# Kernel tuning notes

Hardware: AMD Instinct MI355X
Metric: run time of the kernel (lower is better)

The kernel has to match this reference:

```python
import jax, jax.numpy as jnp
import numpy as np

E = 256
H = 8
DK = E // H


def setup_inputs() -> dict:
    key = jax.random.key(0)
    ks = jax.random.split(key, 16)
    B, NA, NB = 2, 2048, 2048
    x_a = jax.random.normal(ks[0], (B, NA, E), dtype=jnp.float32)
    x_b = jax.random.normal(ks[1], (B, NB, E), dtype=jnp.float32)
    s = 1.0 / np.sqrt(E)  # kaiming-normal-ish scale
    inp = {"x_a": x_a, "x_b": x_b}
    names = ["wq", "wk_a", "wk_b", "wv_a", "wv_b", "w"]
    for i, n in enumerate(names):
        inp[n + "_w"] = jax.random.normal(ks[2 + 2 * i], (E, E), dtype=jnp.float32) * s
        inp[n + "_b"] = jax.random.normal(ks[3 + 2 * i], (E,), dtype=jnp.float32) * 0.01
    return inp


def _linear(x, w, b):
    # torch nn.Linear: y = x @ w.T + b
    return jnp.einsum('bne,fe->bnf', x, w) + b


def _heads(x):
    # [B, N, E] -> [B, H, N, DK]
    B, N, _ = x.shape
    return x.reshape(B, N, H, DK).transpose(0, 2, 1, 3)


def reference(x_a, x_b, wq_w, wq_b, wk_a_w, wk_a_b, wk_b_w, wk_b_b,
              wv_a_w, wv_a_b, wv_b_w, wv_b_b, w_w, w_b):
    B, NA, _ = x_a.shape
    q = _heads(_linear(x_a, wq_w, wq_b))          # [B,H,NA,DK]
    k_a = _heads(_linear(x_a, wk_a_w, wk_a_b))    # [B,H,NA,DK]
    v_a = _heads(_linear(x_a, wv_a_w, wv_a_b))
    k_b = _heads(_linear(x_b, wk_b_w, wk_b_b))    # [B,H,NB,DK]
    v_b = _heads(_linear(x_b, wv_b_w, wv_b_b))
    k = jnp.concatenate([k_a, k_b], axis=2)       # [B,H,NA+NB,DK]
    v = jnp.concatenate([v_a, v_b], axis=2)
    scores = jnp.einsum('bhqd,bhkd->bhqk', q, k) / jnp.sqrt(jnp.float32(DK))
    p = jax.nn.softmax(scores, axis=-1)           # [B,H,NA,NA+NB]
    z = jnp.einsum('bhqk,bhkd->bhqd', p, v)       # [B,H,NA,DK]
    z = z.transpose(0, 2, 1, 3).reshape(B, NA, E)
    out = _linear(z, w_w, w_b) + x_a
    return out
```

## Files before the change

### kernel.cpp

```cpp
#include <hip/hip_runtime.h>
#include <cstdint>

typedef short bf16x8 __attribute__((ext_vector_type(8)));
typedef float f32x4 __attribute__((ext_vector_type(4)));
typedef unsigned short u16;
typedef unsigned int u32;

#define DEVI static __device__ __forceinline__


DEVI u16 f2bf(float f) {
  u32 x = __builtin_bit_cast(u32, f);
  x += 0x7fffu + ((x >> 16) & 1u);
  return (u16)(x >> 16);
}

DEVI u32 pack_bf2(float lo, float hi) {
  return (u32)f2bf(lo) | ((u32)f2bf(hi) << 16);
}

DEVI u32 cvt_pk_bf16(float lo, float hi) {
  u32 r;
  asm("v_cvt_pk_bf16_f32 %0, %1, %2" : "=v"(r) : "v"(lo), "v"(hi));
  return r;
}

DEVI f32x4 mfma16(bf16x8 a, bf16x8 b, f32x4 c) {
  return __builtin_amdgcn_mfma_f32_16x16x32_bf16(a, b, c, 0, 0, 0);
}

DEVI void load_lds16(const void* g, void* l) {
  __builtin_amdgcn_global_load_lds(
      (const __attribute__((address_space(1))) u32*)g,
      (__attribute__((address_space(3))) u32*)l, 16, 0, 0);
}

#define CSCALE 0.2550351f

DEVI int rho(int k) {
  return ((k >> 5) << 5) | (((k >> 2) & 1) << 4) | (((k >> 3) & 3) << 2) | (k & 3);
}

__global__ __launch_bounds__(256) void convert_kernel(
    const float* __restrict__ xa, const float* __restrict__ xb,
    const float* __restrict__ w0, const float* __restrict__ w1,
    const float* __restrict__ w2, const float* __restrict__ w3,
    const float* __restrict__ w4, const float* __restrict__ w5,
    u16* __restrict__ dst) {
  int i = (int)(blockIdx.x * 256u + threadIdx.x) * 8;
  const float* s;
  if (i < 1048576) {
    s = xa + i;
  } else if (i < 2097152) {
    s = xb + (i - 1048576);
  } else {
    int t = i - 2097152;
    int j = t >> 16, o = t & 65535;
    s = (j == 0 ? w0 : j == 1 ? w1 : j == 2 ? w2 : j == 3 ? w3 : j == 4 ? w4 : w5) + o;
  }
  float4 a = *(const float4*)s;
  float4 b = *(const float4*)(s + 4);
  uint4 o4;
  o4.x = pack_bf2(a.x, a.y);
  o4.y = pack_bf2(a.z, a.w);
  o4.z = pack_bf2(b.x, b.y);
  o4.w = pack_bf2(b.z, b.w);
  *(uint4*)(dst + i) = o4;
}

__global__ __launch_bounds__(256) void proj_kernel(
    const u16* __restrict__ xa_bf, const u16* __restrict__ xb_bf,
    const u16* __restrict__ wbase,
    const float* __restrict__ b0, const float* __restrict__ b1,
    const float* __restrict__ b2, const float* __restrict__ b3,
    const float* __restrict__ b4,
    u16* __restrict__ Qo, u16* __restrict__ Ko, u16* __restrict__ Vo) {
  int job = blockIdx.z;
  const u16* A = (job <= 2) ? xa_bf : xb_bf;
  const u16* W = wbase + job * 65536;
  const float* bias = job == 0 ? b0 : job == 1 ? b1 : job == 2 ? b2 : job == 3 ? b3 : b4;
  int mode = (job == 0) ? 0 : (job == 1 || job == 3) ? 1 : 2;
  int soff = (job >= 3) ? 2048 : 0;

  int tid = threadIdx.x, wid = tid >> 6, lane = tid & 63, g = lane >> 4, c = lane & 15;
  int m0 = blockIdx.x * 64, n0 = blockIdx.y * 64;
  const u16* Ap = A + (m0 + wid * 16 + c) * 256 + g * 8;
  const u16* Wp = W + (n0 + c) * 256 + g * 8;
  f32x4 acc[4] = {};
#pragma unroll
  for (int kk = 0; kk < 256; kk += 32) {
    bf16x8 af = *(const bf16x8*)(Ap + kk);
#pragma unroll
    for (int nt = 0; nt < 4; ++nt) {
      bf16x8 bfr = *(const bf16x8*)(Wp + nt * 4096 + kk);
      acc[nt] = mfma16(af, bfr, acc[nt]);
    }
  }
#pragma unroll
  for (int nt = 0; nt < 4; ++nt) {
    int f = n0 + nt * 16 + c;
    float bv = bias[f];
    int h = f >> 5, d = f & 31;
#pragma unroll
    for (int r = 0; r < 4; ++r) {
      int m = m0 + wid * 16 + g * 4 + r;
      int bq = m >> 11, n = m & 2047;
      int bh = bq * 8 + h;
      float y = acc[nt][r] + bv;
      if (mode == 0) {
        Qo[(bh * 2048 + n) * 32 + d] = f2bf(y * CSCALE);
      } else if (mode == 1) {
        int nk = soff + n;
        int pr = (nk & ~63) | rho(nk & 63);
        Ko[((size_t)bh * 4096 + pr) * 32 + d] = f2bf(y);
      } else {
        int nk = soff + n;
        Vo[(size_t)bh * 131072 + (nk >> 6) * 2048 + ((nk >> 3) & 7) * 256 +
           d * 8 + (nk & 7)] = f2bf(y);
      }
    }
  }
}

__global__ __launch_bounds__(256) void attn_kernel(
    const u16* __restrict__ Q, const u16* __restrict__ K,
    const u16* __restrict__ Vt, float* __restrict__ Zp, float* __restrict__ S) {
  __shared__ __align__(16) unsigned char sbuf[24576];
  int bid = blockIdx.x;
  int xcd = bid & 7, slot = bid >> 3;
  int bh = (xcd << 1) | (slot & 1);
  int rem = slot >> 1;
  int ks = rem & 1, qi = rem >> 1;
  int tid = threadIdx.x, wid = tid >> 6, lane = tid & 63;
  int g = lane >> 4, c = lane & 15;
  int qbase = qi * 64 + wid * 16;

  const unsigned char* Kb =
      (const unsigned char*)K + ((size_t)bh * 4096 + ks * 2048) * 64;
  const unsigned char* Vb =
      (const unsigned char*)Vt + (size_t)bh * 262144 + (size_t)ks * 131072;

  bf16x8 qf = *(const bf16x8*)(Q + ((size_t)bh * 2048 + qbase + c) * 32 + g * 8);

  int kaddr = c * 64 + ((g ^ ((c >> 1) & 3)) << 4);
  int vaddr = g * 512 + c * 16;

  int o = wid * 1024 + (lane << 4);
  int ko_src = o ^ (((o >> 7) & 3) << 4);

  f32x4 z0 = {}, z1 = {};
  float lsum = 0.f;

  load_lds16(Kb + ko_src, sbuf + wid * 1024);
  load_lds16(Vb + o, sbuf + 12288 + wid * 1024);

  int cur = 0;
  for (int t = 0; t < 32; ++t) {
    int nxt = cur + 1;
    if (nxt == 3) nxt = 0;
    if (t + 1 < 32) {
      load_lds16(Kb + (t + 1) * 4096 + ko_src, sbuf + nxt * 4096 + wid * 1024);
      load_lds16(Vb + (t + 1) * 4096 + o, sbuf + 12288 + nxt * 4096 + wid * 1024);
      __builtin_amdgcn_sched_barrier(0);
      asm volatile("s_waitcnt vmcnt(2)" ::: "memory");
    } else {
      __builtin_amdgcn_sched_barrier(0);
      asm volatile("s_waitcnt vmcnt(0)" ::: "memory");
    }
    __builtin_amdgcn_s_barrier();
    __builtin_amdgcn_sched_barrier(0);

    const unsigned char* kbuf = sbuf + cur * 4096;
    const unsigned char* vbuf = sbuf + 12288 + cur * 4096;

    bf16x8 kf0 = *(const bf16x8*)(kbuf + kaddr);
    bf16x8 kf1 = *(const bf16x8*)(kbuf + kaddr + 1024);
    bf16x8 kf2 = *(const bf16x8*)(kbuf + kaddr + 2048);
    bf16x8 kf3 = *(const bf16x8*)(kbuf + kaddr + 3072);
    bf16x8 vf00 = *(const bf16x8*)(vbuf + vaddr);
    bf16x8 vf01 = *(const bf16x8*)(vbuf + vaddr + 2048);
    bf16x8 vf10 = *(const bf16x8*)(vbuf + vaddr + 256);
    bf16x8 vf11 = *(const bf16x8*)(vbuf + vaddr + 2048 + 256);

    f32x4 zz = {};
    __builtin_amdgcn_s_setprio(1);
    f32x4 s0 = mfma16(kf0, qf, zz);
    f32x4 s1 = mfma16(kf1, qf, zz);
    f32x4 s2 = mfma16(kf2, qf, zz);
    f32x4 s3 = mfma16(kf3, qf, zz);
    __builtin_amdgcn_s_setprio(0);

    float e0[4], e1[4], e2[4], e3[4];
#pragma unroll
    for (int r = 0; r < 4; ++r) {
      e0[r] = __builtin_amdgcn_exp2f(s0[r]);
      e1[r] = __builtin_amdgcn_exp2f(s1[r]);
      e2[r] = __builtin_amdgcn_exp2f(s2[r]);
      e3[r] = __builtin_amdgcn_exp2f(s3[r]);
    }
    lsum += ((e0[0] + e0[1]) + (e0[2] + e0[3])) + ((e1[0] + e1[1]) + (e1[2] + e1[3])) +
            ((e2[0] + e2[1]) + (e2[2] + e2[3])) + ((e3[0] + e3[1]) + (e3[2] + e3[3]));

    union { u32 u[4]; bf16x8 v; } A0, A1;
    A0.u[0] = cvt_pk_bf16(e0[0], e0[1]);
    A0.u[1] = cvt_pk_bf16(e0[2], e0[3]);
    A0.u[2] = cvt_pk_bf16(e1[0], e1[1]);
    A0.u[3] = cvt_pk_bf16(e1[2], e1[3]);
    A1.u[0] = cvt_pk_bf16(e2[0], e2[1]);
    A1.u[1] = cvt_pk_bf16(e2[2], e2[3]);
    A1.u[2] = cvt_pk_bf16(e3[0], e3[1]);
    A1.u[3] = cvt_pk_bf16(e3[2], e3[3]);

    __builtin_amdgcn_s_setprio(1);
    z0 = mfma16(A0.v, vf00, z0);
    z0 = mfma16(A1.v, vf01, z0);
    z1 = mfma16(A0.v, vf10, z1);
    z1 = mfma16(A1.v, vf11, z1);
    __builtin_amdgcn_s_setprio(0);
    cur = nxt;
  }

  lsum += __shfl_xor(lsum, 16);
  lsum += __shfl_xor(lsum, 32);

  size_t zrow = ((size_t)ks * 16 + bh) * 2048;
  if (lane < 16) S[zrow + qbase + lane] = lsum;
#pragma unroll
  for (int r = 0; r < 4; ++r) {
    int m = qbase + g * 4 + r;
    float* zp = Zp + (zrow + m) * 32;
    zp[c] = z0[r];
    zp[16 + c] = z1[r];
  }
}

__global__ __launch_bounds__(256) void out_kernel(
    const float* __restrict__ Zp, const float* __restrict__ S,
    const u16* __restrict__ W, const float* __restrict__ bias,
    const float* __restrict__ resid, float* __restrict__ out) {
  int tid = threadIdx.x, wid = tid >> 6, lane = tid & 63, g = lane >> 4, c = lane & 15;
  int m0 = blockIdx.x * 16;
  int mrow = m0 + c;
  int bq = mrow >> 11, n = mrow & 2047;
  const u16* Wp = W + (wid * 64 + c) * 256 + g * 8;
  f32x4 acc[4] = {};
#pragma unroll
  for (int h = 0; h < 8; ++h) {
    int bh = bq * 8 + h;
    const float* za = Zp + ((size_t)bh * 2048 + n) * 32 + g * 8;
    const float* zb = za + (size_t)16 * 2048 * 32;
    float4 a0 = *(const float4*)za;
    float4 a1 = *(const float4*)(za + 4);
    float4 b0 = *(const float4*)zb;
    float4 b1 = *(const float4*)(zb + 4);
    float inv = 1.0f / (S[(size_t)bh * 2048 + n] + S[(size_t)(16 + bh) * 2048 + n]);
    union { u32 u[4]; bf16x8 v; } cv;
    cv.u[0] = pack_bf2((a0.x + b0.x) * inv, (a0.y + b0.y) * inv);
    cv.u[1] = pack_bf2((a0.z + b0.z) * inv, (a0.w + b0.w) * inv);
    cv.u[2] = pack_bf2((a1.x + b1.x) * inv, (a1.y + b1.y) * inv);
    cv.u[3] = pack_bf2((a1.z + b1.z) * inv, (a1.w + b1.w) * inv);
    bf16x8 af = cv.v;
#pragma unroll
    for (int nt = 0; nt < 4; ++nt) {
      bf16x8 bfr = *(const bf16x8*)(Wp + nt * 4096 + h * 32);
      acc[nt] = mfma16(af, bfr, acc[nt]);
    }
  }
#pragma unroll
  for (int nt = 0; nt < 4; ++nt) {
    int f = wid * 64 + nt * 16 + c;
    float bv = bias[f];
#pragma unroll
    for (int r = 0; r < 4; ++r) {
      int m = m0 + g * 4 + r;
      out[(size_t)m * 256 + f] = acc[nt][r] + bv + resid[(size_t)m * 256 + f];
    }
  }
}

extern "C" void kernel_launch(void* const* d_in, const int* in_sizes, int n_in,
                              void* d_out, int out_size, void* d_ws, size_t ws_size,
                              hipStream_t stream) {
  const float* xa = (const float*)d_in[0];
  const float* xb = (const float*)d_in[1];
  const float* wq_w = (const float*)d_in[2];
  const float* wq_b = (const float*)d_in[3];
  const float* wka_w = (const float*)d_in[4];
  const float* wka_b = (const float*)d_in[5];
  const float* wkb_w = (const float*)d_in[6];
  const float* wkb_b = (const float*)d_in[7];
  const float* wva_w = (const float*)d_in[8];
  const float* wva_b = (const float*)d_in[9];
  const float* wvb_w = (const float*)d_in[10];
  const float* wvb_b = (const float*)d_in[11];
  const float* w_w = (const float*)d_in[12];
  const float* w_b = (const float*)d_in[13];

  u16* ws = (u16*)d_ws;
  u16* xa_bf = ws;
  u16* xb_bf = ws + 1048576;
  u16* wbf = ws + 2097152;
  u16* Qb = ws + 2490368;
  u16* Kb = ws + 3538944;
  u16* Vtb = ws + 5636096;
  float* Zp = (float*)(ws + 7733248);
  float* S = (float*)((char*)d_ws + 23855104);

  convert_kernel<<<1216, 256, 0, stream>>>(xa, xb, wq_w, wka_w, wva_w, wkb_w,
                                           wvb_w, w_w, ws);
  proj_kernel<<<dim3(64, 4, 5), 256, 0, stream>>>(
      xa_bf, xb_bf, wbf, wq_b, wka_b, wva_b, wkb_b, wvb_b, Qb, Kb, Vtb);
  attn_kernel<<<1024, 256, 0, stream>>>(Qb, Kb, Vtb, Zp, S);
  out_kernel<<<256, 256, 0, stream>>>(Zp, S, wbf + 5 * 65536, w_b, xa,
                                      (float*)d_out);
}
```

Before: 78.35 us.

## Fuse activation conversion into projection, split attention keys four ways, MFMA row sums

Activations are no longer pre-converted to bf16 in a separate pass. The projection kernel now reads fp32 inputs and converts them in registers, so the convert kernel only handles weights. The attention kernel splits keys into four chunks instead of two, doubling the block count, and switches to a 4-deep LDS ring with prefetch distance two. Softmax row sums are now computed with an extra MFMA against a ones vector instead of VALU adds and shuffles. The output kernel merges four partials and splits the output columns across two blocks, at the cost of more partial-sum traffic and reduction work.

New measurement: 88.84 us. 1.13x slower.

```diff
diff --git a/kernel.cpp b/kernel.cpp
--- a/kernel.cpp
+++ b/kernel.cpp
@@ -42,22 +42,14 @@
 }
 
 __global__ __launch_bounds__(256) void convert_kernel(
-    const float* __restrict__ xa, const float* __restrict__ xb,
     const float* __restrict__ w0, const float* __restrict__ w1,
     const float* __restrict__ w2, const float* __restrict__ w3,
     const float* __restrict__ w4, const float* __restrict__ w5,
     u16* __restrict__ dst) {
   int i = (int)(blockIdx.x * 256u + threadIdx.x) * 8;
-  const float* s;
-  if (i < 1048576) {
-    s = xa + i;
-  } else if (i < 2097152) {
-    s = xb + (i - 1048576);
-  } else {
-    int t = i - 2097152;
-    int j = t >> 16, o = t & 65535;
-    s = (j == 0 ? w0 : j == 1 ? w1 : j == 2 ? w2 : j == 3 ? w3 : j == 4 ? w4 : w5) + o;
-  }
+  int j = i >> 16, oo = i & 65535;
+  const float* s =
+      (j == 0 ? w0 : j == 1 ? w1 : j == 2 ? w2 : j == 3 ? w3 : j == 4 ? w4 : w5) + oo;
   float4 a = *(const float4*)s;
   float4 b = *(const float4*)(s + 4);
   uint4 o4;
@@ -69,14 +61,14 @@
 }
 
 __global__ __launch_bounds__(256) void proj_kernel(
-    const u16* __restrict__ xa_bf, const u16* __restrict__ xb_bf,
+    const float* __restrict__ xa, const float* __restrict__ xb,
     const u16* __restrict__ wbase,
     const float* __restrict__ b0, const float* __restrict__ b1,
     const float* __restrict__ b2, const float* __restrict__ b3,
     const float* __restrict__ b4,
     u16* __restrict__ Qo, u16* __restrict__ Ko, u16* __restrict__ Vo) {
   int job = blockIdx.z;
-  const u16* A = (job <= 2) ? xa_bf : xb_bf;
+  const float* A = (job <= 2) ? xa : xb;
   const u16* W = wbase + job * 65536;
   const float* bias = job == 0 ? b0 : job == 1 ? b1 : job == 2 ? b2 : job == 3 ? b3 : b4;
   int mode = (job == 0) ? 0 : (job == 1 || job == 3) ? 1 : 2;
@@ -84,16 +76,22 @@
 
   int tid = threadIdx.x, wid = tid >> 6, lane = tid & 63, g = lane >> 4, c = lane & 15;
   int m0 = blockIdx.x * 64, n0 = blockIdx.y * 64;
-  const u16* Ap = A + (m0 + wid * 16 + c) * 256 + g * 8;
+  const float* Ap = A + (size_t)(m0 + wid * 16 + c) * 256 + g * 8;
   const u16* Wp = W + (n0 + c) * 256 + g * 8;
   f32x4 acc[4] = {};
 #pragma unroll
   for (int kk = 0; kk < 256; kk += 32) {
-    bf16x8 af = *(const bf16x8*)(Ap + kk);
+    float4 x0 = *(const float4*)(Ap + kk);
+    float4 x1 = *(const float4*)(Ap + kk + 4);
+    union { u32 u[4]; bf16x8 v; } af;
+    af.u[0] = cvt_pk_bf16(x0.x, x0.y);
+    af.u[1] = cvt_pk_bf16(x0.z, x0.w);
+    af.u[2] = cvt_pk_bf16(x1.x, x1.y);
+    af.u[3] = cvt_pk_bf16(x1.z, x1.w);
 #pragma unroll
     for (int nt = 0; nt < 4; ++nt) {
       bf16x8 bfr = *(const bf16x8*)(Wp + nt * 4096 + kk);
-      acc[nt] = mfma16(af, bfr, acc[nt]);
+      acc[nt] = mfma16(af.v, bfr, acc[nt]);
     }
   }
 #pragma unroll
@@ -108,7 +106,7 @@
       int bh = bq * 8 + h;
       float y = acc[nt][r] + bv;
       if (mode == 0) {
-        Qo[(bh * 2048 + n) * 32 + d] = f2bf(y * CSCALE);
+        Qo[((size_t)bh * 2048 + n) * 32 + d] = f2bf(y * CSCALE);
       } else if (mode == 1) {
         int nk = soff + n;
         int pr = (nk & ~63) | rho(nk & 63);
@@ -125,20 +123,20 @@
 __global__ __launch_bounds__(256) void attn_kernel(
     const u16* __restrict__ Q, const u16* __restrict__ K,
     const u16* __restrict__ Vt, float* __restrict__ Zp, float* __restrict__ S) {
-  __shared__ __align__(16) unsigned char sbuf[24576];
+  __shared__ __align__(16) unsigned char sbuf[32768];
   int bid = blockIdx.x;
   int xcd = bid & 7, slot = bid >> 3;
   int bh = (xcd << 1) | (slot & 1);
   int rem = slot >> 1;
-  int ks = rem & 1, qi = rem >> 1;
+  int ks = rem & 3, qi = rem >> 2;
   int tid = threadIdx.x, wid = tid >> 6, lane = tid & 63;
   int g = lane >> 4, c = lane & 15;
   int qbase = qi * 64 + wid * 16;
 
   const unsigned char* Kb =
-      (const unsigned char*)K + ((size_t)bh * 4096 + ks * 2048) * 64;
+      (const unsigned char*)K + ((size_t)bh * 4096 + ks * 1024) * 64;
   const unsigned char* Vb =
-      (const unsigned char*)Vt + (size_t)bh * 262144 + (size_t)ks * 131072;
+      (const unsigned char*)Vt + (size_t)bh * 262144 + (size_t)ks * 65536;
 
   bf16x8 qf = *(const bf16x8*)(Q + ((size_t)bh * 2048 + qbase + c) * 32 + g * 8);
 
@@ -148,19 +146,25 @@
   int o = wid * 1024 + (lane << 4);
   int ko_src = o ^ (((o >> 7) & 3) << 4);
 
-  f32x4 z0 = {}, z1 = {};
-  float lsum = 0.f;
+  const u32 one2 = 0x3F803F80u;
+  union { u32 u[4]; bf16x8 v; } ones;
+  ones.u[0] = one2; ones.u[1] = one2; ones.u[2] = one2; ones.u[3] = one2;
+
+  f32x4 z0 = {}, z1 = {}, zs = {};
 
   load_lds16(Kb + ko_src, sbuf + wid * 1024);
-  load_lds16(Vb + o, sbuf + 12288 + wid * 1024);
-
-  int cur = 0;
-  for (int t = 0; t < 32; ++t) {
-    int nxt = cur + 1;
-    if (nxt == 3) nxt = 0;
-    if (t + 1 < 32) {
-      load_lds16(Kb + (t + 1) * 4096 + ko_src, sbuf + nxt * 4096 + wid * 1024);
-      load_lds16(Vb + (t + 1) * 4096 + o, sbuf + 12288 + nxt * 4096 + wid * 1024);
+  load_lds16(Vb + o, sbuf + 16384 + wid * 1024);
+  load_lds16(Kb + 4096 + ko_src, sbuf + 4096 + wid * 1024);
+  load_lds16(Vb + 4096 + o, sbuf + 16384 + 4096 + wid * 1024);
+
+  for (int t = 0; t < 16; ++t) {
+    if (t < 14) {
+      int b2 = (t + 2) & 3;
+      load_lds16(Kb + (t + 2) * 4096 + ko_src, sbuf + b2 * 4096 + wid * 1024);
+      load_lds16(Vb + (t + 2) * 4096 + o, sbuf + 16384 + b2 * 4096 + wid * 1024);
+      __builtin_amdgcn_sched_barrier(0);
+      asm volatile("s_waitcnt vmcnt(4)" ::: "memory");
+    } else if (t == 14) {
       __builtin_amdgcn_sched_barrier(0);
       asm volatile("s_waitcnt vmcnt(2)" ::: "memory");
     } else {
@@ -170,8 +174,8 @@
     __builtin_amdgcn_s_barrier();
     __builtin_amdgcn_sched_barrier(0);
 
-    const unsigned char* kbuf = sbuf + cur * 4096;
-    const unsigned char* vbuf = sbuf + 12288 + cur * 4096;
+    const unsigned char* kbuf = sbuf + (t & 3) * 4096;
+    const unsigned char* vbuf = sbuf + 16384 + (t & 3) * 4096;
 
     bf16x8 kf0 = *(const bf16x8*)(kbuf + kaddr);
     bf16x8 kf1 = *(const bf16x8*)(kbuf + kaddr + 1024);
@@ -198,8 +202,6 @@
       e2[r] = __builtin_amdgcn_exp2f(s2[r]);
       e3[r] = __builtin_amdgcn_exp2f(s3[r]);
     }
-    lsum += ((e0[0] + e0[1]) + (e0[2] + e0[3])) + ((e1[0] + e1[1]) + (e1[2] + e1[3])) +
-            ((e2[0] + e2[1]) + (e2[2] + e2[3])) + ((e3[0] + e3[1]) + (e3[2] + e3[3]));
 
     union { u32 u[4]; bf16x8 v; } A0, A1;
     A0.u[0] = cvt_pk_bf16(e0[0], e0[1]);
@@ -216,15 +218,16 @@
     z0 = mfma16(A1.v, vf01, z0);
     z1 = mfma16(A0.v, vf10, z1);
     z1 = mfma16(A1.v, vf11, z1);
+    zs = mfma16(A0.v, ones.v, zs);
+    zs = mfma16(A1.v, ones.v, zs);
     __builtin_amdgcn_s_setprio(0);
-    cur = nxt;
-  }
-
-  lsum += __shfl_xor(lsum, 16);
-  lsum += __shfl_xor(lsum, 32);
+  }
 
   size_t zrow = ((size_t)ks * 16 + bh) * 2048;
-  if (lane < 16) S[zrow + qbase + lane] = lsum;
+  if (c == 0) {
+#pragma unroll
+    for (int r = 0; r < 4; ++r) S[zrow + qbase + g * 4 + r] = zs[r];
+  }
 #pragma unroll
   for (int r = 0; r < 4; ++r) {
     int m = qbase + g * 4 + r;
@@ -242,33 +245,53 @@
   int m0 = blockIdx.x * 16;
   int mrow = m0 + c;
   int bq = mrow >> 11, n = mrow & 2047;
-  const u16* Wp = W + (wid * 64 + c) * 256 + g * 8;
-  f32x4 acc[4] = {};
+  int nb = blockIdx.y * 128 + wid * 32;
+  const u16* Wp = W + (size_t)(nb + c) * 256 + g * 8;
+
+  float inv[8];
+#pragma unroll
+  for (int h = 0; h < 8; ++h) {
+    size_t sb = (size_t)(bq * 8 + h) * 2048 + n;
+    float t = (S[sb] + S[sb + 32768]) + (S[sb + 65536] + S[sb + 98304]);
+    inv[h] = __builtin_amdgcn_rcpf(t);
+  }
+
+  f32x4 acc[2] = {};
 #pragma unroll
   for (int h = 0; h < 8; ++h) {
     int bh = bq * 8 + h;
-    const float* za = Zp + ((size_t)bh * 2048 + n) * 32 + g * 8;
-    const float* zb = za + (size_t)16 * 2048 * 32;
-    float4 a0 = *(const float4*)za;
-    float4 a1 = *(const float4*)(za + 4);
-    float4 b0 = *(const float4*)zb;
-    float4 b1 = *(const float4*)(zb + 4);
-    float inv = 1.0f / (S[(size_t)bh * 2048 + n] + S[(size_t)(16 + bh) * 2048 + n]);
-    union { u32 u[4]; bf16x8 v; } cv;
-    cv.u[0] = pack_bf2((a0.x + b0.x) * inv, (a0.y + b0.y) * inv);
-    cv.u[1] = pack_bf2((a0.z + b0.z) * inv, (a0.w + b0.w) * inv);
-    cv.u[2] = pack_bf2((a1.x + b1.x) * inv, (a1.y + b1.y) * inv);
-    cv.u[3] = pack_bf2((a1.z + b1.z) * inv, (a1.w + b1.w) * inv);
-    bf16x8 af = cv.v;
-#pragma unroll
-    for (int nt = 0; nt < 4; ++nt) {
+    const float* zp = Zp + ((size_t)bh * 2048 + n) * 32 + g * 8;
+    float4 a0 = *(const float4*)zp;
+    float4 a1 = *(const float4*)(zp + 4);
+    float4 b0 = *(const float4*)(zp + 1048576);
+    float4 b1 = *(const float4*)(zp + 1048576 + 4);
+    float4 c0 = *(const float4*)(zp + 2097152);
+    float4 c1 = *(const float4*)(zp + 2097152 + 4);
+    float4 d0 = *(const float4*)(zp + 3145728);
+    float4 d1 = *(const float4*)(zp + 3145728 + 4);
+    float iv = inv[h];
+    float e0 = ((a0.x + b0.x) + (c0.x + d0.x)) * iv;
+    float e1 = ((a0.y + b0.y) + (c0.y + d0.y)) * iv;
+    float e2 = ((a0.z + b0.z) + (c0.z + d0.z)) * iv;
+    float e3 = ((a0.w + b0.w) + (c0.w + d0.w)) * iv;
+    float e4 = ((a1.x + b1.x) + (c1.x + d1.x)) * iv;
+    float e5 = ((a1.y + b1.y) + (c1.y + d1.y)) * iv;
+    float e6 = ((a1.z + b1.z) + (c1.z + d1.z)) * iv;
+    float e7 = ((a1.w + b1.w) + (c1.w + d1.w)) * iv;
+    union { u32 u[4]; bf16x8 v; } af;
+    af.u[0] = cvt_pk_bf16(e0, e1);
+    af.u[1] = cvt_pk_bf16(e2, e3);
+    af.u[2] = cvt_pk_bf16(e4, e5);
+    af.u[3] = cvt_pk_bf16(e6, e7);
+#pragma unroll
+    for (int nt = 0; nt < 2; ++nt) {
       bf16x8 bfr = *(const bf16x8*)(Wp + nt * 4096 + h * 32);
-      acc[nt] = mfma16(af, bfr, acc[nt]);
-    }
-  }
-#pragma unroll
-  for (int nt = 0; nt < 4; ++nt) {
-    int f = wid * 64 + nt * 16 + c;
+      acc[nt] = mfma16(af.v, bfr, acc[nt]);
+    }
+  }
+#pragma unroll
+  for (int nt = 0; nt < 2; ++nt) {
+    int f = nb + nt * 16 + c;
     float bv = bias[f];
 #pragma unroll
     for (int r = 0; r < 4; ++r) {
@@ -297,20 +320,18 @@
   const float* w_b = (const float*)d_in[13];
 
   u16* ws = (u16*)d_ws;
-  u16* xa_bf = ws;
-  u16* xb_bf = ws + 1048576;
-  u16* wbf = ws + 2097152;
-  u16* Qb = ws + 2490368;
-  u16* Kb = ws + 3538944;
-  u16* Vtb = ws + 5636096;
-  float* Zp = (float*)(ws + 7733248);
-  float* S = (float*)((char*)d_ws + 23855104);
-
-  convert_kernel<<<1216, 256, 0, stream>>>(xa, xb, wq_w, wka_w, wva_w, wkb_w,
-                                           wvb_w, w_w, ws);
+  u16* wbf = ws;
+  u16* Qb = ws + 393216;
+  u16* Kb = ws + 1441792;
+  u16* Vtb = ws + 3538944;
+  float* Zp = (float*)(ws + 5636096);
+  float* S = Zp + 4194304;
+
+  convert_kernel<<<192, 256, 0, stream>>>(wq_w, wka_w, wva_w, wkb_w, wvb_w,
+                                          w_w, wbf);
   proj_kernel<<<dim3(64, 4, 5), 256, 0, stream>>>(
-      xa_bf, xb_bf, wbf, wq_b, wka_b, wva_b, wkb_b, wvb_b, Qb, Kb, Vtb);
-  attn_kernel<<<1024, 256, 0, stream>>>(Qb, Kb, Vtb, Zp, S);
-  out_kernel<<<256, 256, 0, stream>>>(Zp, S, wbf + 5 * 65536, w_b, xa,
-                                      (float*)d_out);
-}
+      xa, xb, wbf, wq_b, wka_b, wva_b, wkb_b, wvb_b, Qb, Kb, Vtb);
+  attn_kernel<<<2048, 256, 0, stream>>>(Qb, Kb, Vtb, Zp, S);
+  out_kernel<<<dim3(256, 2), 256, 0, stream>>>(Zp, S, wbf + 5 * 65536, w_b, xa,
+                                               (float*)d_out);
+}
```
